# Optimization experiments

Hardware: AMD Instinct MI355X
Metric: run time of the kernel (lower is better)

The kernel has to match this reference:

```python
import jax, jax.numpy as jnp
import numpy as np

DISTANCE_W = 1.0
ANGLE_W = 1.0
EPS = 1e-12  # matches F.normalize eps


def setup_inputs() -> dict:
    key = jax.random.key(0)
    k1, k2 = jax.random.split(key)
    student_emb = jax.random.normal(k1, (1024, 512), dtype=jnp.float32)
    teacher_emb = jax.random.normal(k2, (1024, 512), dtype=jnp.float32)
    return {"student_emb": student_emb, "teacher_emb": teacher_emb}


def _pairwise_similarity(emb):
    # F.normalize(emb, dim=1) then emb @ emb.T -> [N, N] cosine similarity
    norm = jnp.maximum(jnp.linalg.norm(emb, axis=1, keepdims=True), EPS)
    en = emb / norm
    return en @ en.T


def _angle_similarity(emb):
    # ||e_i - e_j||^2 for all pairs, computed via the GEMM expansion
    # (same math as the N x N x D broadcast in the original, no O(N^2 D) tensor)
    sq = jnp.sum(emb * emb, axis=1)  # [N]
    gram = emb @ emb.T               # [N, N]
    return sq[:, None] + sq[None, :] - 2.0 * gram


def reference(student_emb, teacher_emb):
    loss_dist = jnp.mean((_pairwise_similarity(student_emb) - _pairwise_similarity(teacher_emb)) ** 2)
    loss_angle = jnp.mean((_angle_similarity(student_emb) - _angle_similarity(teacher_emb)) ** 2)
    return DISTANCE_W * loss_dist + ANGLE_W * loss_angle
```

## Files before the change

### kernel.cpp

```cpp
#include <hip/hip_runtime.h>

typedef short short8 __attribute__((ext_vector_type(8)));
typedef float f32x4 __attribute__((ext_vector_type(4)));

#define DD  512
#define LDT 72


__global__ void init_kernel(float* ws) {
    ws[0] = 0.0f;
    ((unsigned int*)ws)[1] = 0u;
}

__device__ __forceinline__ short to_bf16(float f) {
    unsigned int u = __float_as_uint(f);
    u += 0x7FFFu + ((u >> 16) & 1u);
    return (short)(u >> 16);
}

__device__ __forceinline__ short8 pack8(float4 a, float4 b) {
    short8 r;
    r[0] = to_bf16(a.x); r[1] = to_bf16(a.y); r[2] = to_bf16(a.z); r[3] = to_bf16(a.w);
    r[4] = to_bf16(b.x); r[5] = to_bf16(b.y); r[6] = to_bf16(b.z); r[7] = to_bf16(b.w);
    return r;
}

__device__ __forceinline__ float dot4(float4 v) {
    return v.x*v.x + v.y*v.y + v.z*v.z + v.w*v.w;
}

__global__ __launch_bounds__(256, 2) void rkd_mfma_kernel(const float* __restrict__ S,
                                                          const float* __restrict__ T,
                                                          float* __restrict__ ws,
                                                          float* __restrict__ out) {
    __shared__ short AS[64][LDT], AT[64][LDT];
    __shared__ short BS[32][LDT], BT[32][LDT];
    __shared__ float sqAS[64], sqAT[64], sqBS[32], sqBT[32];
    __shared__ float wsum[4];

    const int t = threadIdx.x;
    const int I = (blockIdx.x >> 5) * 64;
    const int J = (blockIdx.x & 31) * 32;

    const int r8 = t >> 3;
    const int co = (t & 7) * 8;

    const float* pA1s = S + (size_t)(I + r8) * DD + co;
    const float* pA2s = S + (size_t)(I + 32 + r8) * DD + co;
    const float* pA1t = T + (size_t)(I + r8) * DD + co;
    const float* pA2t = T + (size_t)(I + 32 + r8) * DD + co;
    const float* pBs  = S + (size_t)(J + r8) * DD + co;
    const float* pBt  = T + (size_t)(J + r8) * DD + co;

    const int w    = t >> 6;
    const int L    = t & 63;
    const int m    = L & 15;
    const int quad = L >> 4;
    const int arow = w * 16 + m;
    const int koff = quad * 8;

    f32x4 aS0 = {0,0,0,0}, aS1 = {0,0,0,0};
    f32x4 aT0 = {0,0,0,0}, aT1 = {0,0,0,0};
    float p1s = 0, p2s = 0, p1t = 0, p2t = 0, pbs = 0, pbt = 0;

    for (int k0 = 0; k0 < DD; k0 += 64) {
        float4 A1sa = *(const float4*)(pA1s + k0);
        float4 A1sb = *(const float4*)(pA1s + k0 + 4);
        float4 A2sa = *(const float4*)(pA2s + k0);
        float4 A2sb = *(const float4*)(pA2s + k0 + 4);
        float4 A1ta = *(const float4*)(pA1t + k0);
        float4 A1tb = *(const float4*)(pA1t + k0 + 4);
        float4 A2ta = *(const float4*)(pA2t + k0);
        float4 A2tb = *(const float4*)(pA2t + k0 + 4);
        float4 Bsa  = *(const float4*)(pBs + k0);
        float4 Bsb  = *(const float4*)(pBs + k0 + 4);
        float4 Bta  = *(const float4*)(pBt + k0);
        float4 Btb  = *(const float4*)(pBt + k0 + 4);

        p1s += dot4(A1sa) + dot4(A1sb);
        p2s += dot4(A2sa) + dot4(A2sb);
        p1t += dot4(A1ta) + dot4(A1tb);
        p2t += dot4(A2ta) + dot4(A2tb);
        pbs += dot4(Bsa) + dot4(Bsb);
        pbt += dot4(Bta) + dot4(Btb);

        __syncthreads();

        *(short8*)&AS[r8][co]      = pack8(A1sa, A1sb);
        *(short8*)&AS[32 + r8][co] = pack8(A2sa, A2sb);
        *(short8*)&AT[r8][co]      = pack8(A1ta, A1tb);
        *(short8*)&AT[32 + r8][co] = pack8(A2ta, A2tb);
        *(short8*)&BS[r8][co]      = pack8(Bsa, Bsb);
        *(short8*)&BT[r8][co]      = pack8(Bta, Btb);

        __syncthreads();

        #pragma unroll
        for (int ks = 0; ks < 2; ++ks) {
            const int kb = ks * 32 + koff;
            short8 af_s = *(const short8*)&AS[arow][kb];
            short8 af_t = *(const short8*)&AT[arow][kb];
            short8 b_s0 = *(const short8*)&BS[m][kb];
            short8 b_s1 = *(const short8*)&BS[16 + m][kb];
            short8 b_t0 = *(const short8*)&BT[m][kb];
            short8 b_t1 = *(const short8*)&BT[16 + m][kb];
            aS0 = __builtin_amdgcn_mfma_f32_16x16x32_bf16(af_s, b_s0, aS0, 0, 0, 0);
            aS1 = __builtin_amdgcn_mfma_f32_16x16x32_bf16(af_s, b_s1, aS1, 0, 0, 0);
            aT0 = __builtin_amdgcn_mfma_f32_16x16x32_bf16(af_t, b_t0, aT0, 0, 0, 0);
            aT1 = __builtin_amdgcn_mfma_f32_16x16x32_bf16(af_t, b_t1, aT1, 0, 0, 0);
        }
    }

    #pragma unroll
    for (int msk = 1; msk <= 4; msk <<= 1) {
        p1s += __shfl_xor(p1s, msk);
        p2s += __shfl_xor(p2s, msk);
        p1t += __shfl_xor(p1t, msk);
        p2t += __shfl_xor(p2t, msk);
        pbs += __shfl_xor(pbs, msk);
        pbt += __shfl_xor(pbt, msk);
    }
    if ((t & 7) == 0) {
        sqAS[r8] = p1s;  sqAS[32 + r8] = p2s;
        sqAT[r8] = p1t;  sqAT[32 + r8] = p2t;
        sqBS[r8] = pbs;  sqBT[r8] = pbt;
    }
    __syncthreads();

    float js0 = sqBS[m],      js1 = sqBS[16 + m];
    float jt0 = sqBT[m],      jt1 = sqBT[16 + m];
    float rjs0 = 1.0f / fmaxf(sqrtf(js0), 1e-12f);
    float rjs1 = 1.0f / fmaxf(sqrtf(js1), 1e-12f);
    float rjt0 = 1.0f / fmaxf(sqrtf(jt0), 1e-12f);
    float rjt1 = 1.0f / fmaxf(sqrtf(jt1), 1e-12f);

    float local = 0.0f;
    const int ib = w * 16 + quad * 4;
    #pragma unroll
    for (int reg = 0; reg < 4; ++reg) {
        const int r = ib + reg;
        float is = sqAS[r], it = sqAT[r];
        float ris = 1.0f / fmaxf(sqrtf(is), 1e-12f);
        float rit = 1.0f / fmaxf(sqrtf(it), 1e-12f);

        float gs0 = aS0[reg], gt0 = aT0[reg];
        float d1 = gs0 * ris * rjs0 - gt0 * rit * rjt0;
        float d2 = (is + js0 - 2.0f * gs0) - (it + jt0 - 2.0f * gt0);
        local += d1 * d1 + d2 * d2;

        float gs1 = aS1[reg], gt1 = aT1[reg];
        float e1 = gs1 * ris * rjs1 - gt1 * rit * rjt1;
        float e2 = (is + js1 - 2.0f * gs1) - (it + jt1 - 2.0f * gt1);
        local += e1 * e1 + e2 * e2;
    }

    #pragma unroll
    for (int off = 32; off > 0; off >>= 1) local += __shfl_down(local, off);
    if (L == 0) wsum[w] = local;
    __syncthreads();

    if (t == 0) {
        float blk = wsum[0] + wsum[1] + wsum[2] + wsum[3];
        atomicAdd(&ws[0], blk);
        __threadfence();
        unsigned int old = atomicAdd((unsigned int*)ws + 1, 1u);
        if (old == 511u) {
            float tot = atomicAdd(&ws[0], 0.0f);
            out[0] = tot * (1.0f / 1048576.0f);
        }
    }
}

extern "C" void kernel_launch(void* const* d_in, const int* in_sizes, int n_in,
                              void* d_out, int out_size, void* d_ws, size_t ws_size,
                              hipStream_t stream) {
    const float* S = (const float*)d_in[0];
    const float* T = (const float*)d_in[1];
    float* ws  = (float*)d_ws;
    float* out = (float*)d_out;

    init_kernel<<<1, 1, 0, stream>>>(ws);
    rkd_mfma_kernel<<<512, 256, 0, stream>>>(S, T, ws, out);
}
```

Before: 84.09 us.

## Pre-convert embeddings to bf16 and stream tiles via global_load_lds with XOR swizzle

Adds a conversion pass that turns each embedding row into bf16 once and precomputes squared norms and reciprocal norms. The tile kernel then loads bf16 tiles directly into LDS with global_load_lds and reads them through an XOR-swizzled layout, so it no longer redoes fp32 loads, conversion and norm reductions per tile. This halves the bytes each tile reads and removes the per-block norm work. The cost is an extra kernel pass and a workspace round trip, and the load and MFMA steps are still not double-buffered.

After: 78.69 us. -6.4%, faster.

```diff
diff --git a/kernel.cpp b/kernel.cpp
--- a/kernel.cpp
+++ b/kernel.cpp
@@ -2,15 +2,10 @@
 
 typedef short short8 __attribute__((ext_vector_type(8)));
 typedef float f32x4 __attribute__((ext_vector_type(4)));
+typedef unsigned short ushort;
 
-#define DD  512
-#define LDT 72
+#define DD 512
 
-
-__global__ void init_kernel(float* ws) {
-    ws[0] = 0.0f;
-    ((unsigned int*)ws)[1] = 0u;
-}
 
 __device__ __forceinline__ short to_bf16(float f) {
     unsigned int u = __float_as_uint(f);
@@ -29,81 +24,87 @@
     return v.x*v.x + v.y*v.y + v.z*v.z + v.w*v.w;
 }
 
-__global__ __launch_bounds__(256, 2) void rkd_mfma_kernel(const float* __restrict__ S,
-                                                          const float* __restrict__ T,
-                                                          float* __restrict__ ws,
+__global__ __launch_bounds__(64) void convert_kernel(const float* __restrict__ S,
+                                                     const float* __restrict__ T,
+                                                     ushort* __restrict__ bf,
+                                                     float* __restrict__ sqarr,
+                                                     float* __restrict__ accw) {
+    const int idx  = blockIdx.x;
+    const int lane = threadIdx.x;
+    const float* src = (idx < 1024) ? (S + (size_t)idx * DD)
+                                    : (T + (size_t)(idx - 1024) * DD);
+    float4 v0 = ((const float4*)src)[lane * 2];
+    float4 v1 = ((const float4*)src)[lane * 2 + 1];
+    *(short8*)(bf + (size_t)idx * DD + lane * 8) = pack8(v0, v1);
+    float s = dot4(v0) + dot4(v1);
+    #pragma unroll
+    for (int off = 32; off > 0; off >>= 1) s += __shfl_down(s, off);
+    if (lane == 0) {
+        sqarr[idx]        = s;
+        sqarr[2048 + idx] = 1.0f / fmaxf(sqrtf(s), 1e-12f);
+        if (idx == 0) { accw[0] = 0.0f; ((unsigned int*)accw)[1] = 0u; }
+    }
+}
+
+__global__ __launch_bounds__(256, 2) void rkd_tile_kernel(const ushort* __restrict__ bf,
+                                                          const float* __restrict__ sqarr,
+                                                          float* __restrict__ accw,
                                                           float* __restrict__ out) {
-    __shared__ short AS[64][LDT], AT[64][LDT];
-    __shared__ short BS[32][LDT], BT[32][LDT];
-    __shared__ float sqAS[64], sqAT[64], sqBS[32], sqBT[32];
+    __shared__ ushort AS[64][64], AT[64][64];
+    __shared__ ushort BS[32][64], BT[32][64];
     __shared__ float wsum[4];
 
     const int t = threadIdx.x;
     const int I = (blockIdx.x >> 5) * 64;
     const int J = (blockIdx.x & 31) * 32;
-
-    const int r8 = t >> 3;
-    const int co = (t & 7) * 8;
-
-    const float* pA1s = S + (size_t)(I + r8) * DD + co;
-    const float* pA2s = S + (size_t)(I + 32 + r8) * DD + co;
-    const float* pA1t = T + (size_t)(I + r8) * DD + co;
-    const float* pA2t = T + (size_t)(I + 32 + r8) * DD + co;
-    const float* pBs  = S + (size_t)(J + r8) * DD + co;
-    const float* pBt  = T + (size_t)(J + r8) * DD + co;
-
-    const int w    = t >> 6;
-    const int L    = t & 63;
-    const int m    = L & 15;
+    const int w = t >> 6;
+    const int L = t & 63;
+    const int m = L & 15;
     const int quad = L >> 4;
     const int arow = w * 16 + m;
-    const int koff = quad * 8;
+
+    const ushort* bS = bf;
+    const ushort* bT = bf + (size_t)1024 * DD;
+
+    const int lrow = L >> 3;
+    const int lchk = (L & 7) ^ lrow;
+    const int lgoff = lrow * DD + lchk * 8;
+
+    const ushort* gtab[6];
+    ushort* ltab[6];
+    #pragma unroll
+    for (int j = 0; j < 6; ++j) {
+        const int q = w * 6 + j;
+        const ushort* gmat; ushort* lmat; int rbase, gbase;
+        if (q < 8)       { gmat = bS; lmat = &AS[0][0]; rbase = q * 8;        gbase = I; }
+        else if (q < 16) { gmat = bT; lmat = &AT[0][0]; rbase = (q - 8) * 8;  gbase = I; }
+        else if (q < 20) { gmat = bS; lmat = &BS[0][0]; rbase = (q - 16) * 8; gbase = J; }
+        else             { gmat = bT; lmat = &BT[0][0]; rbase = (q - 20) * 8; gbase = J; }
+        gtab[j] = gmat + (size_t)(gbase + rbase) * DD + lgoff;
+        ltab[j] = lmat + rbase * 64;
+    }
 
     f32x4 aS0 = {0,0,0,0}, aS1 = {0,0,0,0};
     f32x4 aT0 = {0,0,0,0}, aT1 = {0,0,0,0};
-    float p1s = 0, p2s = 0, p1t = 0, p2t = 0, pbs = 0, pbt = 0;
 
     for (int k0 = 0; k0 < DD; k0 += 64) {
-        float4 A1sa = *(const float4*)(pA1s + k0);
-        float4 A1sb = *(const float4*)(pA1s + k0 + 4);
-        float4 A2sa = *(const float4*)(pA2s + k0);
-        float4 A2sb = *(const float4*)(pA2s + k0 + 4);
-        float4 A1ta = *(const float4*)(pA1t + k0);
-        float4 A1tb = *(const float4*)(pA1t + k0 + 4);
-        float4 A2ta = *(const float4*)(pA2t + k0);
-        float4 A2tb = *(const float4*)(pA2t + k0 + 4);
-        float4 Bsa  = *(const float4*)(pBs + k0);
-        float4 Bsb  = *(const float4*)(pBs + k0 + 4);
-        float4 Bta  = *(const float4*)(pBt + k0);
-        float4 Btb  = *(const float4*)(pBt + k0 + 4);
-
-        p1s += dot4(A1sa) + dot4(A1sb);
-        p2s += dot4(A2sa) + dot4(A2sb);
-        p1t += dot4(A1ta) + dot4(A1tb);
-        p2t += dot4(A2ta) + dot4(A2tb);
-        pbs += dot4(Bsa) + dot4(Bsb);
-        pbt += dot4(Bta) + dot4(Btb);
-
         __syncthreads();
-
-        *(short8*)&AS[r8][co]      = pack8(A1sa, A1sb);
-        *(short8*)&AS[32 + r8][co] = pack8(A2sa, A2sb);
-        *(short8*)&AT[r8][co]      = pack8(A1ta, A1tb);
-        *(short8*)&AT[32 + r8][co] = pack8(A2ta, A2tb);
-        *(short8*)&BS[r8][co]      = pack8(Bsa, Bsb);
-        *(short8*)&BT[r8][co]      = pack8(Bta, Btb);
-
+        #pragma unroll
+        for (int j = 0; j < 6; ++j)
+            __builtin_amdgcn_global_load_lds(
+                (const __attribute__((address_space(1))) void*)(gtab[j] + k0),
+                (__attribute__((address_space(3))) void*)ltab[j], 16, 0, 0);
         __syncthreads();
 
         #pragma unroll
         for (int ks = 0; ks < 2; ++ks) {
-            const int kb = ks * 32 + koff;
-            short8 af_s = *(const short8*)&AS[arow][kb];
-            short8 af_t = *(const short8*)&AT[arow][kb];
-            short8 b_s0 = *(const short8*)&BS[m][kb];
-            short8 b_s1 = *(const short8*)&BS[16 + m][kb];
-            short8 b_t0 = *(const short8*)&BT[m][kb];
-            short8 b_t1 = *(const short8*)&BT[16 + m][kb];
+            const int cs = (((ks * 4 + quad) ^ (m & 7))) * 8;
+            short8 af_s = *(const short8*)&AS[arow][cs];
+            short8 af_t = *(const short8*)&AT[arow][cs];
+            short8 b_s0 = *(const short8*)&BS[m][cs];
+            short8 b_s1 = *(const short8*)&BS[16 + m][cs];
+            short8 b_t0 = *(const short8*)&BT[m][cs];
+            short8 b_t1 = *(const short8*)&BT[16 + m][cs];
             aS0 = __builtin_amdgcn_mfma_f32_16x16x32_bf16(af_s, b_s0, aS0, 0, 0, 0);
             aS1 = __builtin_amdgcn_mfma_f32_16x16x32_bf16(af_s, b_s1, aS1, 0, 0, 0);
             aT0 = __builtin_amdgcn_mfma_f32_16x16x32_bf16(af_t, b_t0, aT0, 0, 0, 0);
@@ -111,37 +112,19 @@
         }
     }
 
-    #pragma unroll
-    for (int msk = 1; msk <= 4; msk <<= 1) {
-        p1s += __shfl_xor(p1s, msk);
-        p2s += __shfl_xor(p2s, msk);
-        p1t += __shfl_xor(p1t, msk);
-        p2t += __shfl_xor(p2t, msk);
-        pbs += __shfl_xor(pbs, msk);
-        pbt += __shfl_xor(pbt, msk);
-    }
-    if ((t & 7) == 0) {
-        sqAS[r8] = p1s;  sqAS[32 + r8] = p2s;
-        sqAT[r8] = p1t;  sqAT[32 + r8] = p2t;
-        sqBS[r8] = pbs;  sqBT[r8] = pbt;
-    }
-    __syncthreads();
-
-    float js0 = sqBS[m],      js1 = sqBS[16 + m];
-    float jt0 = sqBT[m],      jt1 = sqBT[16 + m];
-    float rjs0 = 1.0f / fmaxf(sqrtf(js0), 1e-12f);
-    float rjs1 = 1.0f / fmaxf(sqrtf(js1), 1e-12f);
-    float rjt0 = 1.0f / fmaxf(sqrtf(jt0), 1e-12f);
-    float rjt1 = 1.0f / fmaxf(sqrtf(jt1), 1e-12f);
+    const int j0 = J + m, j1 = J + 16 + m;
+    float js0 = sqarr[j0],        jt0 = sqarr[1024 + j0];
+    float rjs0 = sqarr[2048 + j0], rjt0 = sqarr[3072 + j0];
+    float js1 = sqarr[j1],        jt1 = sqarr[1024 + j1];
+    float rjs1 = sqarr[2048 + j1], rjt1 = sqarr[3072 + j1];
 
     float local = 0.0f;
-    const int ib = w * 16 + quad * 4;
+    const int ib = I + w * 16 + quad * 4;
     #pragma unroll
     for (int reg = 0; reg < 4; ++reg) {
         const int r = ib + reg;
-        float is = sqAS[r], it = sqAT[r];
-        float ris = 1.0f / fmaxf(sqrtf(is), 1e-12f);
-        float rit = 1.0f / fmaxf(sqrtf(it), 1e-12f);
+        float is = sqarr[r],        it = sqarr[1024 + r];
+        float ris = sqarr[2048 + r], rit = sqarr[3072 + r];
 
         float gs0 = aS0[reg], gt0 = aT0[reg];
         float d1 = gs0 * ris * rjs0 - gt0 * rit * rjt0;
@@ -161,11 +144,11 @@
 
     if (t == 0) {
         float blk = wsum[0] + wsum[1] + wsum[2] + wsum[3];
-        atomicAdd(&ws[0], blk);
+        atomicAdd(&accw[0], blk);
         __threadfence();
-        unsigned int old = atomicAdd((unsigned int*)ws + 1, 1u);
+        unsigned int old = atomicAdd((unsigned int*)accw + 1, 1u);
         if (old == 511u) {
-            float tot = atomicAdd(&ws[0], 0.0f);
+            float tot = atomicAdd(&accw[0], 0.0f);
             out[0] = tot * (1.0f / 1048576.0f);
         }
     }
@@ -176,9 +159,11 @@
                               hipStream_t stream) {
     const float* S = (const float*)d_in[0];
     const float* T = (const float*)d_in[1];
-    float* ws  = (float*)d_ws;
-    float* out = (float*)d_out;
+    ushort* bf   = (ushort*)d_ws;
+    float* sqarr = (float*)((char*)d_ws + 2 * 1024 * 1024);
+    float* accw  = sqarr + 4096;
+    float* out   = (float*)d_out;
 
-    init_kernel<<<1, 1, 0, stream>>>(ws);
-    rkd_mfma_kernel<<<512, 256, 0, stream>>>(S, T, ws, out);
+    convert_kernel<<<2048, 64, 0, stream>>>(S, T, bf, sqarr, accw);
+    rkd_tile_kernel<<<512, 256, 0, stream>>>(bf, sqarr, accw, out);
 }
```
